# Performance work log

Measured on AMD Instinct MI355X. Metric: run time of the kernel, lower is better.

## Reference

```python
import jax, jax.numpy as jnp
import numpy as np

UNITS = 1024
B, T = 32, 2048


def setup_inputs() -> dict:
    key = jax.random.key(0)
    ks = jax.random.split(key, 8)
    s = 1.0 / np.sqrt(UNITS)
    return {
        "x": jax.random.normal(ks[0], (B, T, UNITS), dtype=jnp.float32),
        "hidden": jax.random.normal(ks[1], (B, UNITS), dtype=jnp.float32),
        "W1_w": jax.random.uniform(ks[2], (UNITS, UNITS), jnp.float32, -s, s),
        "W1_b": jax.random.uniform(ks[3], (UNITS,), jnp.float32, -s, s),
        "W2_w": jax.random.uniform(ks[4], (UNITS, UNITS), jnp.float32, -s, s),
        "W2_b": jax.random.uniform(ks[5], (UNITS,), jnp.float32, -s, s),
        "V_w": jax.random.uniform(ks[6], (1, UNITS), jnp.float32, -s, s),
        "V_b": jax.random.uniform(ks[7], (1,), jnp.float32, -s, s),
    }


def reference(x, hidden, W1_w, W1_b, W2_w, W2_b, V_w, V_b):
    # hidden.squeeze().unsqueeze(1): [B, U] -> [B, 1, U]
    h = hidden[:, None, :]
    # tanh(W1(x) + W2(hidden)): [B, T, U]
    att = jnp.tanh(
        jnp.einsum("btu,vu->btv", x, W1_w) + W1_b
        + jnp.einsum("bsu,vu->bsv", h, W2_w) + W2_b
    )
    # score = V(att): [B, T, 1]
    score = jnp.einsum("btu,ou->bto", att, V_w) + V_b
    # softmax over T, then squeeze().unsqueeze(1): [B, T, 1] -> [B, 1, T]
    attention_weights = jnp.swapaxes(jax.nn.softmax(score, axis=1), 1, 2)
    # bmm([B,1,T], [B,T,U]) -> [B,1,U]; squeeze().unsqueeze(0) -> [1, B, U]
    context_vector = jnp.matmul(attention_weights, x)[:, 0, :][None, :, :]
    return context_vector, attention_weights
```

## Files before the change

kernel.cpp:

```cpp
#include <hip/hip_runtime.h>
#include <hip/hip_bf16.h>
#include <cstdint>
#include <cstddef>

#define UNITS 1024
#define BDIM 32
#define TDIM 2048
#define M_TOT (BDIM*TDIM)
#define KDIM UNITS
#define NDIM UNITS
#define NPART 8

#define K2LOG2E 2.885390081777927f

typedef __attribute__((ext_vector_type(8))) short bf16x8;
typedef __attribute__((ext_vector_type(8))) unsigned short ushort8;
typedef __attribute__((ext_vector_type(4))) float f32x4;

__device__ __forceinline__ unsigned short f2bf(float f) {
  unsigned u = __float_as_uint(f);
  u += 0x7fffu + ((u >> 16) & 1u);
  return (unsigned short)(u >> 16);
}
__device__ __forceinline__ float bf2f(unsigned short h) {
  return __uint_as_float(((unsigned)h) << 16);
}

__global__ __launch_bounds__(256) void cvt_kernel(const float* __restrict__ src,
                                                  ushort* __restrict__ dst, int n8) {
  int i = blockIdx.x * blockDim.x + threadIdx.x;
  int stride = gridDim.x * blockDim.x;
  const float4* s4 = (const float4*)src;
  ushort8* d8 = (ushort8*)dst;
  for (; i < n8; i += stride) {
    float4 a = s4[2*i], b = s4[2*i+1];
    ushort8 o;
    o[0] = f2bf(a.x); o[1] = f2bf(a.y); o[2] = f2bf(a.z); o[3] = f2bf(a.w);
    o[4] = f2bf(b.x); o[5] = f2bf(b.y); o[6] = f2bf(b.z); o[7] = f2bf(b.w);
    d8[i] = o;
  }
}

__global__ __launch_bounds__(64) void prep_c_kernel(const float* __restrict__ W2w,
                                                    const float* __restrict__ hidden,
                                                    const float* __restrict__ W1b,
                                                    const float* __restrict__ W2b,
                                                    float* __restrict__ c) {
  int v = blockIdx.x;
  int l = threadIdx.x;
  float acc[BDIM];
  #pragma unroll
  for (int b = 0; b < BDIM; b++) acc[b] = 0.f;
  for (int u0 = 0; u0 < UNITS; u0 += 64) {
    float w = W2w[v*UNITS + u0 + l];
    #pragma unroll
    for (int b = 0; b < BDIM; b++) acc[b] += w * hidden[b*UNITS + u0 + l];
  }
  float bias = W1b[v] + W2b[v];
  #pragma unroll
  for (int b = 0; b < BDIM; b++) {
    float s = acc[b];
    #pragma unroll
    for (int off = 32; off > 0; off >>= 1) s += __shfl_xor(s, off);
    if (l == 0) c[b*UNITS + v] = s + bias;
  }
}

__global__ __launch_bounds__(256, 3) void gemm_score_kernel(
    const ushort* __restrict__ A,
    const ushort* __restrict__ W,
    const float* __restrict__ c,
    const float* __restrict__ Vw,
    float* __restrict__ score)
{
  __shared__ ushort As[128*64];
  __shared__ ushort Bs[128*64];
  __shared__ float sred[256];

  const int nt = blockIdx.x & 7;
  const int m0 = (blockIdx.x >> 3) * 128;
  const int n0 = nt * 128;
  const int bb = m0 >> 11;
  const int tid = threadIdx.x;
  const int wave = tid >> 6;
  const int l = tid & 63;
  const int lrow = l & 15;
  const int lq = l >> 4;
  const int wm = (wave >> 1) * 64;
  const int wn = (wave & 1) * 64;

  const int srow = tid >> 3;
  const int s_g  = ((tid & 7) - srow) & 7;
  const int p0 = ((lq + lrow) & 7) * 8;
  const int p1 = (((4 + lq + lrow) & 7)) * 8;
  const int abase = (wm + lrow) * 64;
  const int bbase = (wn + lrow) * 64;

  const ushort* ag0 = A + (size_t)(m0 + srow) * KDIM + s_g * 8;
  const ushort* ag1 = ag0 + (size_t)32 * KDIM;
  const ushort* ag2 = ag0 + (size_t)64 * KDIM;
  const ushort* ag3 = ag0 + (size_t)96 * KDIM;
  const ushort* bg0 = W + (size_t)(n0 + srow) * KDIM + s_g * 8;
  const ushort* bg1 = bg0 + (size_t)32 * KDIM;
  const ushort* bg2 = bg0 + (size_t)64 * KDIM;
  const ushort* bg3 = bg0 + (size_t)96 * KDIM;

  ushort* lA0 = As + wave * 512;
  ushort* lA1 = As + 2048 + wave * 512;
  ushort* lA2 = As + 4096 + wave * 512;
  ushort* lA3 = As + 6144 + wave * 512;
  ushort* lB0 = Bs + wave * 512;
  ushort* lB1 = Bs + 2048 + wave * 512;
  ushort* lB2 = Bs + 4096 + wave * 512;
  ushort* lB3 = Bs + 6144 + wave * 512;

  f32x4 acc[4][4];
  #pragma unroll
  for (int i = 0; i < 4; i++)
    #pragma unroll
    for (int j = 0; j < 4; j++) acc[i][j] = (f32x4)0.f;

  for (int k0 = 0; k0 < KDIM; k0 += 64) {
    __builtin_amdgcn_global_load_lds((const __attribute__((address_space(1))) void*)ag0,
                                     (__attribute__((address_space(3))) void*)lA0, 16, 0, 0);
    __builtin_amdgcn_global_load_lds((const __attribute__((address_space(1))) void*)ag1,
                                     (__attribute__((address_space(3))) void*)lA1, 16, 0, 0);
    __builtin_amdgcn_global_load_lds((const __attribute__((address_space(1))) void*)ag2,
                                     (__attribute__((address_space(3))) void*)lA2, 16, 0, 0);
    __builtin_amdgcn_global_load_lds((const __attribute__((address_space(1))) void*)ag3,
                                     (__attribute__((address_space(3))) void*)lA3, 16, 0, 0);
    __builtin_amdgcn_global_load_lds((const __attribute__((address_space(1))) void*)bg0,
                                     (__attribute__((address_space(3))) void*)lB0, 16, 0, 0);
    __builtin_amdgcn_global_load_lds((const __attribute__((address_space(1))) void*)bg1,
                                     (__attribute__((address_space(3))) void*)lB1, 16, 0, 0);
    __builtin_amdgcn_global_load_lds((const __attribute__((address_space(1))) void*)bg2,
                                     (__attribute__((address_space(3))) void*)lB2, 16, 0, 0);
    __builtin_amdgcn_global_load_lds((const __attribute__((address_space(1))) void*)bg3,
                                     (__attribute__((address_space(3))) void*)lB3, 16, 0, 0);
    ag0 += 64; ag1 += 64; ag2 += 64; ag3 += 64;
    bg0 += 64; bg1 += 64; bg2 += 64; bg3 += 64;
    __syncthreads();
    {
      bf16x8 af[4], bfv[4];
      #pragma unroll
      for (int i = 0; i < 4; i++) af[i] = *(const bf16x8*)(As + abase + i * 1024 + p0);
      #pragma unroll
      for (int j = 0; j < 4; j++) bfv[j] = *(const bf16x8*)(Bs + bbase + j * 1024 + p0);
      #pragma unroll
      for (int i = 0; i < 4; i++)
        #pragma unroll
        for (int j = 0; j < 4; j++)
          acc[i][j] = __builtin_amdgcn_mfma_f32_16x16x32_bf16(af[i], bfv[j], acc[i][j], 0, 0, 0);
    }
    {
      bf16x8 af[4], bfv[4];
      #pragma unroll
      for (int i = 0; i < 4; i++) af[i] = *(const bf16x8*)(As + abase + i * 1024 + p1);
      #pragma unroll
      for (int j = 0; j < 4; j++) bfv[j] = *(const bf16x8*)(Bs + bbase + j * 1024 + p1);
      #pragma unroll
      for (int i = 0; i < 4; i++)
        #pragma unroll
        for (int j = 0; j < 4; j++)
          acc[i][j] = __builtin_amdgcn_mfma_f32_16x16x32_bf16(af[i], bfv[j], acc[i][j], 0, 0, 0);
    }
    __syncthreads();
  }

  float vw4[4], ck4[4];
  float vws = 0.f;
  #pragma unroll
  for (int j = 0; j < 4; j++) {
    int n = n0 + wn + j * 16 + lrow;
    float v = Vw[n];
    vw4[j] = v;
    vws += v;
    ck4[j] = c[bb * NDIM + n] * K2LOG2E;
  }
  float sacc[4][4];
  #pragma unroll
  for (int i = 0; i < 4; i++)
    #pragma unroll
    for (int r = 0; r < 4; r++) sacc[i][r] = 0.f;
  #pragma unroll
  for (int i = 0; i < 4; i++)
    #pragma unroll
    for (int j = 0; j < 4; j++)
      #pragma unroll
      for (int r = 0; r < 4; r++) {
        float t = __builtin_fmaf(acc[i][j][r], K2LOG2E, ck4[j]);
        float e = __builtin_amdgcn_exp2f(t);
        float rr = __builtin_amdgcn_rcpf(e + 1.f);
        sacc[i][r] = __builtin_fmaf(vw4[j], rr, sacc[i][r]);
      }

  #pragma unroll
  for (int i = 0; i < 4; i++)
    #pragma unroll
    for (int r = 0; r < 4; r++) {
      float s = vws - 2.f * sacc[i][r];
      s += __shfl_xor(s, 1);
      s += __shfl_xor(s, 2);
      s += __shfl_xor(s, 4);
      s += __shfl_xor(s, 8);
      if (lrow == 0) sred[wave * 64 + i * 16 + lq * 4 + r] = s;
    }
  __syncthreads();
  if (tid < 128) {
    int hh = tid >> 6;
    int ml = tid & 63;
    float v = sred[hh * 128 + ml] + sred[hh * 128 + 64 + ml];
    score[(size_t)nt * M_TOT + m0 + tid] = v;
  }
}

__global__ __launch_bounds__(256) void softmax_kernel(float* __restrict__ sc,
                                                      float* __restrict__ wout) {
  const int b = blockIdx.x;
  const int tid = threadIdx.x;
  float4* s4 = (float4*)(sc + (size_t)b * TDIM);
  float4 v0 = s4[2*tid], v1 = s4[2*tid+1];
  #pragma unroll
  for (int k = 1; k < NPART; k++) {
    const float4* p4 = (const float4*)(sc + (size_t)k * M_TOT + (size_t)b * TDIM);
    float4 u0 = p4[2*tid], u1 = p4[2*tid+1];
    v0.x += u0.x; v0.y += u0.y; v0.z += u0.z; v0.w += u0.w;
    v1.x += u1.x; v1.y += u1.y; v1.z += u1.z; v1.w += u1.w;
  }
  float mx = fmaxf(fmaxf(fmaxf(v0.x,v0.y),fmaxf(v0.z,v0.w)),
                   fmaxf(fmaxf(v1.x,v1.y),fmaxf(v1.z,v1.w)));
  #pragma unroll
  for (int off = 32; off > 0; off >>= 1) mx = fmaxf(mx, __shfl_xor(mx, off));
  __shared__ float redm[4];
  __shared__ float reds[4];
  if ((tid & 63) == 0) redm[tid >> 6] = mx;
  __syncthreads();
  mx = fmaxf(fmaxf(redm[0], redm[1]), fmaxf(redm[2], redm[3]));
  v0.x = __expf(v0.x - mx); v0.y = __expf(v0.y - mx);
  v0.z = __expf(v0.z - mx); v0.w = __expf(v0.w - mx);
  v1.x = __expf(v1.x - mx); v1.y = __expf(v1.y - mx);
  v1.z = __expf(v1.z - mx); v1.w = __expf(v1.w - mx);
  float sum = v0.x+v0.y+v0.z+v0.w+v1.x+v1.y+v1.z+v1.w;
  #pragma unroll
  for (int off = 32; off > 0; off >>= 1) sum += __shfl_xor(sum, off);
  if ((tid & 63) == 0) reds[tid >> 6] = sum;
  __syncthreads();
  sum = reds[0]+reds[1]+reds[2]+reds[3];
  float inv = 1.f / sum;
  v0.x *= inv; v0.y *= inv; v0.z *= inv; v0.w *= inv;
  v1.x *= inv; v1.y *= inv; v1.z *= inv; v1.w *= inv;
  s4[2*tid] = v0; s4[2*tid+1] = v1;
  float4* w4 = (float4*)(wout + (size_t)b * TDIM);
  w4[2*tid] = v0; w4[2*tid+1] = v1;
}

__global__ __launch_bounds__(256) void context_kernel(const ushort* __restrict__ xb,
                                                      const float* __restrict__ wgt,
                                                      float* __restrict__ ctx) {
  const int uc = blockIdx.x;
  const int b = blockIdx.y;
  const int tid = threadIdx.x;
  __shared__ float wl[TDIM];
  {
    const float4* wsrc = (const float4*)(wgt + (size_t)b * TDIM);
    float4* wdst = (float4*)wl;
    wdst[tid] = wsrc[tid];
    wdst[tid + 256] = wsrc[tid + 256];
  }
  __syncthreads();
  const int ut = tid & 15;
  const int tr = tid >> 4;
  const ushort* xp = xb + (size_t)b * TDIM * UNITS + uc * 128 + ut * 8;
  float a8[8];
  #pragma unroll
  for (int e = 0; e < 8; e++) a8[e] = 0.f;
  for (int t = tr; t < TDIM; t += 64) {
    ushort8 x0 = *(const ushort8*)(xp + (size_t)(t     ) * UNITS);
    ushort8 x1 = *(const ushort8*)(xp + (size_t)(t + 16) * UNITS);
    ushort8 x2 = *(const ushort8*)(xp + (size_t)(t + 32) * UNITS);
    ushort8 x3 = *(const ushort8*)(xp + (size_t)(t + 48) * UNITS);
    float w0 = wl[t], w1 = wl[t+16], w2 = wl[t+32], w3 = wl[t+48];
    #pragma unroll
    for (int e = 0; e < 8; e++) {
      a8[e] += w0 * bf2f(x0[e]);
      a8[e] += w1 * bf2f(x1[e]);
      a8[e] += w2 * bf2f(x2[e]);
      a8[e] += w3 * bf2f(x3[e]);
    }
  }
  #pragma unroll
  for (int e = 0; e < 8; e++) {
    a8[e] += __shfl_xor(a8[e], 16);
    a8[e] += __shfl_xor(a8[e], 32);
  }
  __shared__ float red[512];
  const int wave = tid >> 6;
  const int l = tid & 63;
  if (l < 16) {
    #pragma unroll
    for (int e = 0; e < 8; e++) red[wave * 128 + l * 8 + e] = a8[e];
  }
  __syncthreads();
  if (tid < 128) {
    float v = red[tid] + red[128 + tid] + red[256 + tid] + red[384 + tid];
    ctx[(size_t)b * UNITS + uc * 128 + tid] = v;
  }
}

extern "C" void kernel_launch(void* const* d_in, const int* in_sizes, int n_in,
                              void* d_out, int out_size, void* d_ws, size_t ws_size,
                              hipStream_t stream) {
  const float* x   = (const float*)d_in[0];
  const float* hid = (const float*)d_in[1];
  const float* W1w = (const float*)d_in[2];
  const float* W1b = (const float*)d_in[3];
  const float* W2w = (const float*)d_in[4];
  const float* W2b = (const float*)d_in[5];
  const float* Vw  = (const float*)d_in[6];
  float* out = (float*)d_out;

  char* ws = (char*)d_ws;
  ushort* xb   = (ushort*)ws;
  ushort* w1b  = (ushort*)(ws + (size_t)M_TOT*KDIM*2);
  float*  cbuf = (float*)(ws + (size_t)M_TOT*KDIM*2 + (size_t)NDIM*KDIM*2);
  float*  score= (float*)((char*)cbuf + (size_t)BDIM*NDIM*4);

  cvt_kernel<<<4096, 256, 0, stream>>>(x, xb, M_TOT*KDIM/8);
  cvt_kernel<<<512, 256, 0, stream>>>(W1w, w1b, NDIM*KDIM/8);
  prep_c_kernel<<<NDIM, 64, 0, stream>>>(W2w, hid, W1b, W2b, cbuf);
  gemm_score_kernel<<<M_TOT/128 * NPART, 256, 0, stream>>>(xb, w1b, cbuf, Vw, score);
  softmax_kernel<<<BDIM, 256, 0, stream>>>(score, out + (size_t)BDIM*UNITS);
  context_kernel<<<dim3(8, BDIM), 256, 0, stream>>>(xb, score, out);
}
```

Baseline: 575.3 us.

## Enlarge GEMM tile to 256x256 with double-buffered LDS pipeline

Result: no change. 579.0 us (+0.6%).

```diff
diff --git a/kernel.cpp b/kernel.cpp
--- a/kernel.cpp
+++ b/kernel.cpp
@@ -9,7 +9,7 @@
 #define M_TOT (BDIM*TDIM)
 #define KDIM UNITS
 #define NDIM UNITS
-#define NPART 8
+#define NPART 4
 
 #define K2LOG2E 2.885390081777927f
 
@@ -66,106 +66,119 @@
   }
 }
 
-__global__ __launch_bounds__(256, 3) void gemm_score_kernel(
+#define GLL(g, l) __builtin_amdgcn_global_load_lds(                              \
+    (const __attribute__((address_space(1))) void*)(g),                          \
+    (__attribute__((address_space(3))) void*)(l), 16, 0, 0)
+
+__global__ __launch_bounds__(512, 2) void gemm_score_kernel(
     const ushort* __restrict__ A,
     const ushort* __restrict__ W,
     const float* __restrict__ c,
     const float* __restrict__ Vw,
     float* __restrict__ score)
 {
-  __shared__ ushort As[128*64];
-  __shared__ ushort Bs[128*64];
-  __shared__ float sred[256];
-
-  const int nt = blockIdx.x & 7;
-  const int m0 = (blockIdx.x >> 3) * 128;
-  const int n0 = nt * 128;
+  __shared__ ushort sh[2][2][16384];
+  ushort* shb = &sh[0][0][0];
+
+  const int nt = blockIdx.x & 3;
+  const int m0 = (blockIdx.x >> 2) * 256;
+  const int n0 = nt * 256;
   const int bb = m0 >> 11;
   const int tid = threadIdx.x;
   const int wave = tid >> 6;
   const int l = tid & 63;
   const int lrow = l & 15;
   const int lq = l >> 4;
-  const int wm = (wave >> 1) * 64;
-  const int wn = (wave & 1) * 64;
+  const int wm = (wave >> 2) * 128;
+  const int wn = (wave & 3) * 64;
 
   const int srow = tid >> 3;
   const int s_g  = ((tid & 7) - srow) & 7;
   const int p0 = ((lq + lrow) & 7) * 8;
-  const int p1 = (((4 + lq + lrow) & 7)) * 8;
-  const int abase = (wm + lrow) * 64;
-  const int bbase = (wn + lrow) * 64;
-
-  const ushort* ag0 = A + (size_t)(m0 + srow) * KDIM + s_g * 8;
-  const ushort* ag1 = ag0 + (size_t)32 * KDIM;
-  const ushort* ag2 = ag0 + (size_t)64 * KDIM;
-  const ushort* ag3 = ag0 + (size_t)96 * KDIM;
-  const ushort* bg0 = W + (size_t)(n0 + srow) * KDIM + s_g * 8;
-  const ushort* bg1 = bg0 + (size_t)32 * KDIM;
-  const ushort* bg2 = bg0 + (size_t)64 * KDIM;
-  const ushort* bg3 = bg0 + (size_t)96 * KDIM;
-
-  ushort* lA0 = As + wave * 512;
-  ushort* lA1 = As + 2048 + wave * 512;
-  ushort* lA2 = As + 4096 + wave * 512;
-  ushort* lA3 = As + 6144 + wave * 512;
-  ushort* lB0 = Bs + wave * 512;
-  ushort* lB1 = Bs + 2048 + wave * 512;
-  ushort* lB2 = Bs + 4096 + wave * 512;
-  ushort* lB3 = Bs + 6144 + wave * 512;
-
-  f32x4 acc[4][4];
-  #pragma unroll
-  for (int i = 0; i < 4; i++)
+  const int p1 = ((lq + lrow + 4) & 7) * 8;
+  const int aoff = (wm + lrow) * 64;
+  const int boff = (wn + lrow) * 64;
+
+  const ushort* gA0 = A + (size_t)(m0 + srow) * KDIM + s_g * 8;
+  const ushort* gA1 = gA0 + (size_t)64 * KDIM;
+  const ushort* gA2 = gA0 + (size_t)128 * KDIM;
+  const ushort* gA3 = gA0 + (size_t)192 * KDIM;
+  const ushort* gB0 = W + (size_t)(n0 + srow) * KDIM + s_g * 8;
+  const ushort* gB1 = gB0 + (size_t)64 * KDIM;
+  const ushort* gB2 = gB0 + (size_t)128 * KDIM;
+  const ushort* gB3 = gB0 + (size_t)192 * KDIM;
+
+  f32x4 acc[8][4];
+  #pragma unroll
+  for (int i = 0; i < 8; i++)
     #pragma unroll
     for (int j = 0; j < 4; j++) acc[i][j] = (f32x4)0.f;
 
-  for (int k0 = 0; k0 < KDIM; k0 += 64) {
-    __builtin_amdgcn_global_load_lds((const __attribute__((address_space(1))) void*)ag0,
-                                     (__attribute__((address_space(3))) void*)lA0, 16, 0, 0);
-    __builtin_amdgcn_global_load_lds((const __attribute__((address_space(1))) void*)ag1,
-                                     (__attribute__((address_space(3))) void*)lA1, 16, 0, 0);
-    __builtin_amdgcn_global_load_lds((const __attribute__((address_space(1))) void*)ag2,
-                                     (__attribute__((address_space(3))) void*)lA2, 16, 0, 0);
-    __builtin_amdgcn_global_load_lds((const __attribute__((address_space(1))) void*)ag3,
-                                     (__attribute__((address_space(3))) void*)lA3, 16, 0, 0);
-    __builtin_amdgcn_global_load_lds((const __attribute__((address_space(1))) void*)bg0,
-                                     (__attribute__((address_space(3))) void*)lB0, 16, 0, 0);
-    __builtin_amdgcn_global_load_lds((const __attribute__((address_space(1))) void*)bg1,
-                                     (__attribute__((address_space(3))) void*)lB1, 16, 0, 0);
-    __builtin_amdgcn_global_load_lds((const __attribute__((address_space(1))) void*)bg2,
-                                     (__attribute__((address_space(3))) void*)lB2, 16, 0, 0);
-    __builtin_amdgcn_global_load_lds((const __attribute__((address_space(1))) void*)bg3,
-                                     (__attribute__((address_space(3))) void*)lB3, 16, 0, 0);
-    ag0 += 64; ag1 += 64; ag2 += 64; ag3 += 64;
-    bg0 += 64; bg1 += 64; bg2 += 64; bg3 += 64;
-    __syncthreads();
+  auto STAGE = [&](int buf) {
+    ushort* dA = shb + buf * 32768 + wave * 512;
+    ushort* dB = dA + 16384;
+    GLL(gA0, dA);          GLL(gA1, dA + 4096);
+    GLL(gA2, dA + 8192);   GLL(gA3, dA + 12288);
+    GLL(gB0, dB);          GLL(gB1, dB + 4096);
+    GLL(gB2, dB + 8192);   GLL(gB3, dB + 12288);
+    gA0 += 64; gA1 += 64; gA2 += 64; gA3 += 64;
+    gB0 += 64; gB1 += 64; gB2 += 64; gB3 += 64;
+  };
+
+  auto COMPUTE = [&](int buf) {
+    const ushort* Ab = shb + buf * 32768;
+    const ushort* Bb = Ab + 16384;
     {
-      bf16x8 af[4], bfv[4];
-      #pragma unroll
-      for (int i = 0; i < 4; i++) af[i] = *(const bf16x8*)(As + abase + i * 1024 + p0);
-      #pragma unroll
-      for (int j = 0; j < 4; j++) bfv[j] = *(const bf16x8*)(Bs + bbase + j * 1024 + p0);
-      #pragma unroll
-      for (int i = 0; i < 4; i++)
+      bf16x8 a[8], b[4];
+      #pragma unroll
+      for (int i = 0; i < 8; i++) a[i] = *(const bf16x8*)(Ab + aoff + i * 1024 + p0);
+      #pragma unroll
+      for (int j = 0; j < 4; j++) b[j] = *(const bf16x8*)(Bb + boff + j * 1024 + p0);
+      __builtin_amdgcn_s_setprio(1);
+      #pragma unroll
+      for (int i = 0; i < 8; i++)
         #pragma unroll
         for (int j = 0; j < 4; j++)
-          acc[i][j] = __builtin_amdgcn_mfma_f32_16x16x32_bf16(af[i], bfv[j], acc[i][j], 0, 0, 0);
+          acc[i][j] = __builtin_amdgcn_mfma_f32_16x16x32_bf16(a[i], b[j], acc[i][j], 0, 0, 0);
+      __builtin_amdgcn_s_setprio(0);
     }
     {
-      bf16x8 af[4], bfv[4];
-      #pragma unroll
-      for (int i = 0; i < 4; i++) af[i] = *(const bf16x8*)(As + abase + i * 1024 + p1);
-      #pragma unroll
-      for (int j = 0; j < 4; j++) bfv[j] = *(const bf16x8*)(Bs + bbase + j * 1024 + p1);
-      #pragma unroll
-      for (int i = 0; i < 4; i++)
+      bf16x8 a[8], b[4];
+      #pragma unroll
+      for (int i = 0; i < 8; i++) a[i] = *(const bf16x8*)(Ab + aoff + i * 1024 + p1);
+      #pragma unroll
+      for (int j = 0; j < 4; j++) b[j] = *(const bf16x8*)(Bb + boff + j * 1024 + p1);
+      __builtin_amdgcn_s_setprio(1);
+      #pragma unroll
+      for (int i = 0; i < 8; i++)
         #pragma unroll
         for (int j = 0; j < 4; j++)
-          acc[i][j] = __builtin_amdgcn_mfma_f32_16x16x32_bf16(af[i], bfv[j], acc[i][j], 0, 0, 0);
+          acc[i][j] = __builtin_amdgcn_mfma_f32_16x16x32_bf16(a[i], b[j], acc[i][j], 0, 0, 0);
+      __builtin_amdgcn_s_setprio(0);
     }
-    __syncthreads();
-  }
+  };
+
+  STAGE(0);
+  STAGE(1);
+  asm volatile("s_waitcnt vmcnt(8)" ::: "memory");
+  __builtin_amdgcn_s_barrier();
+  int cur = 0;
+  #pragma unroll 1
+  for (int kt = 0; kt < 14; ++kt) {
+    COMPUTE(cur);
+    asm volatile("s_waitcnt lgkmcnt(0)" ::: "memory");
+    __builtin_amdgcn_s_barrier();
+    STAGE(cur);
+    asm volatile("s_waitcnt vmcnt(8)" ::: "memory");
+    __builtin_amdgcn_s_barrier();
+    cur ^= 1;
+  }
+  COMPUTE(cur);
+  asm volatile("s_waitcnt lgkmcnt(0)" ::: "memory");
+  __builtin_amdgcn_s_barrier();
+  asm volatile("s_waitcnt vmcnt(0)" ::: "memory");
+  __builtin_amdgcn_s_barrier();
+  COMPUTE(cur ^ 1);
 
   float vw4[4], ck4[4];
   float vws = 0.f;
@@ -177,13 +190,13 @@
     vws += v;
     ck4[j] = c[bb * NDIM + n] * K2LOG2E;
   }
-  float sacc[4][4];
-  #pragma unroll
-  for (int i = 0; i < 4; i++)
+  float sacc[8][4];
+  #pragma unroll
+  for (int i = 0; i < 8; i++)
     #pragma unroll
     for (int r = 0; r < 4; r++) sacc[i][r] = 0.f;
   #pragma unroll
-  for (int i = 0; i < 4; i++)
+  for (int i = 0; i < 8; i++)
     #pragma unroll
     for (int j = 0; j < 4; j++)
       #pragma unroll
@@ -194,8 +207,9 @@
         sacc[i][r] = __builtin_fmaf(vw4[j], rr, sacc[i][r]);
       }
 
-  #pragma unroll
-  for (int i = 0; i < 4; i++)
+  float* sred = (float*)shb;
+  #pragma unroll
+  for (int i = 0; i < 8; i++)
     #pragma unroll
     for (int r = 0; r < 4; r++) {
       float s = vws - 2.f * sacc[i][r];
@@ -203,13 +217,14 @@
       s += __shfl_xor(s, 2);
       s += __shfl_xor(s, 4);
       s += __shfl_xor(s, 8);
-      if (lrow == 0) sred[wave * 64 + i * 16 + lq * 4 + r] = s;
+      if (lrow == 0) sred[wave * 128 + i * 16 + lq * 4 + r] = s;
     }
   __syncthreads();
-  if (tid < 128) {
-    int hh = tid >> 6;
-    int ml = tid & 63;
-    float v = sred[hh * 128 + ml] + sred[hh * 128 + 64 + ml];
+  if (tid < 256) {
+    int mh = tid >> 7;
+    int ml = tid & 127;
+    float v = sred[mh * 512 + ml] + sred[mh * 512 + 128 + ml]
+            + sred[mh * 512 + 256 + ml] + sred[mh * 512 + 384 + ml];
     score[(size_t)nt * M_TOT + m0 + tid] = v;
   }
 }
@@ -328,7 +343,7 @@
   cvt_kernel<<<4096, 256, 0, stream>>>(x, xb, M_TOT*KDIM/8);
   cvt_kernel<<<512, 256, 0, stream>>>(W1w, w1b, NDIM*KDIM/8);
   prep_c_kernel<<<NDIM, 64, 0, stream>>>(W2w, hid, W1b, W2b, cbuf);
-  gemm_score_kernel<<<M_TOT/128 * NPART, 256, 0, stream>>>(xb, w1b, cbuf, Vw, score);
+  gemm_score_kernel<<<M_TOT/256 * NPART, 512, 0, stream>>>(xb, w1b, cbuf, Vw, score);
   softmax_kernel<<<BDIM, 256, 0, stream>>>(score, out + (size_t)BDIM*UNITS);
   context_kernel<<<dim3(8, BDIM), 256, 0, stream>>>(xb, score, out);
 }
```
